# Kernel optimization log

Hardware: AMD Instinct MI355X
Metric: run time of the kernel (lower is better)

## Reference

```python
import jax, jax.numpy as jnp
import numpy as np

B, S, E, H = 4, 2048, 1024, 16
D = E // H  # head dim


def setup_inputs() -> dict:
    key = jax.random.key(0)
    ks = jax.random.split(key, 6)
    sc = 1.0 / np.sqrt(E)
    return {
        "x":  jax.random.normal(ks[0], (B, S, E), dtype=jnp.float32),
        "Wk": jax.random.normal(ks[1], (E, E), dtype=jnp.float32) * sc,
        "Wq": jax.random.normal(ks[2], (E, E), dtype=jnp.float32) * sc,
        "Wv": jax.random.normal(ks[3], (E, E), dtype=jnp.float32) * sc,
        "Wo": jax.random.normal(ks[4], (E, E), dtype=jnp.float32) * sc,
        "bo": jax.random.normal(ks[5], (E,), dtype=jnp.float32) * sc,
    }


def reference(x, Wk, Wq, Wv, Wo, bo):
    b, s, e = x.shape
    # torch Linear: y = x @ W.T (weights are [out, in])
    K = x @ Wk.T
    Q = x @ Wq.T
    _V_unused = x @ Wv.T  # computed in source but discarded (V = Q.view bug)
    # split heads: [b, s, H, D] -> [b, H, s, D]
    Kh = K.reshape(b, s, H, D).transpose(0, 2, 1, 3)
    Qh = Q.reshape(b, s, H, D).transpose(0, 2, 1, 3)
    Vh = Qh  # faithful to source: V = Q.view(...)
    # scaled dot product, scaled by sqrt(embedding_size) as in source
    scores = jnp.einsum('bhqd,bhkd->bhqk', Qh, Kh) / jnp.sqrt(jnp.float32(e))
    causal = jnp.tril(jnp.ones((s, s), dtype=bool))
    scores = jnp.where(causal, scores, -jnp.inf)
    probs = jax.nn.softmax(scores, axis=-1)
    attn = jnp.einsum('bhqk,bhkd->bhqd', probs, Vh)
    attn = attn.transpose(0, 2, 1, 3).reshape(b, s, e)
    return attn @ Wo.T + bo
```

## Files before the change

### kernel.cpp

```cpp
#include <hip/hip_runtime.h>
#include <hip/hip_bf16.h>

#define PB 4
#define PS 2048
#define PE 1024
#define PH 16
#define PD 64

typedef __attribute__((ext_vector_type(8))) short bf16x8;
typedef __attribute__((ext_vector_type(4))) float f32x4;
typedef const __attribute__((address_space(1))) unsigned int* gas_t;
typedef __attribute__((address_space(3))) unsigned int* las_t;

__device__ __forceinline__ unsigned short f2bf(float f) {
  union { float f; unsigned int u; } v;
  v.f = f;
  unsigned int u = v.u;
  u += 0x7fffu + ((u >> 16) & 1u);
  return (unsigned short)(u >> 16);
}

__device__ __forceinline__ f32x4 mfma16(bf16x8 a, bf16x8 b, f32x4 c) {
  return __builtin_amdgcn_mfma_f32_16x16x32_bf16(a, b, c, 0, 0, 0);
}

#define CVT_GROUPS ((PB * PS * PE + 3 * PE * PE) / 4)
#define CVT_BLOCKS (CVT_GROUPS / 256)
__global__ __launch_bounds__(256) void cvt_kernel(
    const float* __restrict__ x, const float* __restrict__ wk,
    const float* __restrict__ wq, const float* __restrict__ wo,
    unsigned short* __restrict__ xb, unsigned short* __restrict__ wkb,
    unsigned short* __restrict__ wqb, unsigned short* __restrict__ wob) {
  const long long NX = (long long)PB * PS * PE;
  const long long NW = (long long)PE * PE;
  long long i = ((long long)blockIdx.x * 256 + threadIdx.x) * 4;
  const float* src;
  unsigned short* dst;
  long long off;
  if (i < NX)               { src = x;  dst = xb;  off = i; }
  else if (i < NX + NW)     { src = wk; dst = wkb; off = i - NX; }
  else if (i < NX + 2 * NW) { src = wq; dst = wqb; off = i - NX - NW; }
  else                      { src = wo; dst = wob; off = i - NX - 2 * NW; }
  float4 v = *(const float4*)(src + off);
  ushort4 o;
  o.x = f2bf(v.x); o.y = f2bf(v.y); o.z = f2bf(v.z); o.w = f2bf(v.w);
  *(ushort4*)(dst + off) = o;
}

__global__ __launch_bounds__(256) void gemm_qknt(
    const unsigned short* __restrict__ A, const unsigned short* __restrict__ Bq,
    const unsigned short* __restrict__ Bk,
    unsigned short* __restrict__ QT, unsigned short* __restrict__ Kb) {
  const int K = PE, N = PE;
  __shared__ __attribute__((aligned(16))) unsigned short As[128 * 64];
  __shared__ __attribute__((aligned(16))) unsigned short Bs[128 * 64];
  const int tid = threadIdx.x;
  const int wave = tid >> 6, lane = tid & 63;
  const int quad = lane >> 4, ln = lane & 15;
  const int m0 = blockIdx.y * 128, n0 = blockIdx.x * 128;
  const int wm = (wave >> 1) * 64, wn = (wave & 1) * 64;
  const int isK = blockIdx.z;
  const unsigned short* __restrict__ Bsrc = isK ? Bk : Bq;

  f32x4 acc[4][4];
#pragma unroll
  for (int i = 0; i < 4; ++i)
#pragma unroll
    for (int j = 0; j < 4; ++j)
#pragma unroll
      for (int r = 0; r < 4; ++r) acc[i][j][r] = 0.f;

  for (int k0 = 0; k0 < K; k0 += 64) {
#pragma unroll
    for (int it = 0; it < 4; ++it) {
      const int idx = it * 256 + tid;
      const int row = idx >> 3, ch = idx & 7;
      const int gch = ch ^ (row & 7);
      __builtin_amdgcn_global_load_lds(
          (gas_t)(const void*)(A + (size_t)(m0 + row) * K + k0 + gch * 8),
          (las_t)(void*)((char*)As + idx * 16), 16, 0, 0);
      __builtin_amdgcn_global_load_lds(
          (gas_t)(const void*)(Bsrc + (size_t)(n0 + row) * K + k0 + gch * 8),
          (las_t)(void*)((char*)Bs + idx * 16), 16, 0, 0);
    }
    __syncthreads();
#pragma unroll
    for (int kc = 0; kc < 2; ++kc) {
      bf16x8 af[4], bfr[4];
#pragma unroll
      for (int t = 0; t < 4; ++t) {
        const int ra = wm + t * 16 + ln;
        const int rb = wn + t * 16 + ln;
        af[t]  = *(const bf16x8*)(As + ra * 64 + ((kc * 4 + quad) ^ (ra & 7)) * 8);
        bfr[t] = *(const bf16x8*)(Bs + rb * 64 + ((kc * 4 + quad) ^ (rb & 7)) * 8);
      }
      if (!isK) {
#pragma unroll
        for (int mt = 0; mt < 4; ++mt)
#pragma unroll
          for (int nt = 0; nt < 4; ++nt)
            acc[mt][nt] = mfma16(af[mt], bfr[nt], acc[mt][nt]);
      } else {
#pragma unroll
        for (int mt = 0; mt < 4; ++mt)
#pragma unroll
          for (int nt = 0; nt < 4; ++nt)
            acc[mt][nt] = mfma16(bfr[nt], af[mt], acc[mt][nt]);
      }
    }
    __syncthreads();
  }

  const float CEXP = 0.045084220f;
  if (!isK) {
#pragma unroll
    for (int mt = 0; mt < 4; ++mt)
#pragma unroll
      for (int nt = 0; nt < 4; ++nt) {
        const int row = m0 + wm + mt * 16 + quad * 4;
        const int col = n0 + wn + nt * 16 + ln;
        const int b = row >> 11, s = row & 2047;
        const int h = col >> 6, d = col & 63;
        ushort4 ov;
        ov.x = f2bf(acc[mt][nt][0]); ov.y = f2bf(acc[mt][nt][1]);
        ov.z = f2bf(acc[mt][nt][2]); ov.w = f2bf(acc[mt][nt][3]);
        *(ushort4*)(QT + (((size_t)(b * PH + h) * PD + d) * PS + s)) = ov;
      }
  } else {
#pragma unroll
    for (int mt = 0; mt < 4; ++mt)
#pragma unroll
      for (int nt = 0; nt < 4; ++nt) {
        const int krow = m0 + wm + mt * 16 + ln;
        const int kcol = n0 + wn + nt * 16 + quad * 4;
        ushort4 kv;
        kv.x = f2bf(acc[mt][nt][0] * CEXP); kv.y = f2bf(acc[mt][nt][1] * CEXP);
        kv.z = f2bf(acc[mt][nt][2] * CEXP); kv.w = f2bf(acc[mt][nt][3] * CEXP);
        *(ushort4*)(Kb + (size_t)krow * N + kcol) = kv;
      }
  }
}

__global__ __launch_bounds__(256) void gemm_out(
    const unsigned short* __restrict__ A, const unsigned short* __restrict__ Bm,
    const float* __restrict__ bias, float* __restrict__ Cf) {
  const int K = PE, N = PE;
  __shared__ __attribute__((aligned(16))) unsigned short As[64 * 64];
  __shared__ __attribute__((aligned(16))) unsigned short Bs[128 * 64];
  const int tid = threadIdx.x;
  const int wave = tid >> 6, lane = tid & 63;
  const int quad = lane >> 4, ln = lane & 15;
  const int m0 = blockIdx.y * 64, n0 = blockIdx.x * 128;
  const int wm = (wave >> 1) * 32, wn = (wave & 1) * 64;

  f32x4 acc[2][4];
#pragma unroll
  for (int i = 0; i < 2; ++i)
#pragma unroll
    for (int j = 0; j < 4; ++j)
#pragma unroll
      for (int r = 0; r < 4; ++r) acc[i][j][r] = 0.f;

  for (int k0 = 0; k0 < K; k0 += 64) {
#pragma unroll
    for (int it = 0; it < 2; ++it) {
      const int idx = it * 256 + tid;
      const int row = idx >> 3, ch = idx & 7;
      const int gch = ch ^ (row & 7);
      __builtin_amdgcn_global_load_lds(
          (gas_t)(const void*)(A + (size_t)(m0 + row) * K + k0 + gch * 8),
          (las_t)(void*)((char*)As + idx * 16), 16, 0, 0);
    }
#pragma unroll
    for (int it = 0; it < 4; ++it) {
      const int idx = it * 256 + tid;
      const int row = idx >> 3, ch = idx & 7;
      const int gch = ch ^ (row & 7);
      __builtin_amdgcn_global_load_lds(
          (gas_t)(const void*)(Bm + (size_t)(n0 + row) * K + k0 + gch * 8),
          (las_t)(void*)((char*)Bs + idx * 16), 16, 0, 0);
    }
    __syncthreads();
#pragma unroll
    for (int kc = 0; kc < 2; ++kc) {
      bf16x8 af[2], bfr[4];
#pragma unroll
      for (int t = 0; t < 2; ++t) {
        const int ra = wm + t * 16 + ln;
        af[t] = *(const bf16x8*)(As + ra * 64 + ((kc * 4 + quad) ^ (ra & 7)) * 8);
      }
#pragma unroll
      for (int t = 0; t < 4; ++t) {
        const int rb = wn + t * 16 + ln;
        bfr[t] = *(const bf16x8*)(Bs + rb * 64 + ((kc * 4 + quad) ^ (rb & 7)) * 8);
      }
#pragma unroll
      for (int mt = 0; mt < 2; ++mt)
#pragma unroll
        for (int nt = 0; nt < 4; ++nt)
          acc[mt][nt] = mfma16(bfr[nt], af[mt], acc[mt][nt]);
    }
    __syncthreads();
  }

#pragma unroll
  for (int mt = 0; mt < 2; ++mt) {
#pragma unroll
    for (int nt = 0; nt < 4; ++nt) {
      const int row  = m0 + wm + mt * 16 + ln;
      const int colb = n0 + wn + nt * 16 + quad * 4;
      const float4 bv = *(const float4*)(bias + colb);
      float4 ov;
      ov.x = acc[mt][nt][0] + bv.x; ov.y = acc[mt][nt][1] + bv.y;
      ov.z = acc[mt][nt][2] + bv.z; ov.w = acc[mt][nt][3] + bv.w;
      *(float4*)(Cf + (size_t)row * N + colb) = ov;
    }
  }
}

__global__ __launch_bounds__(256) void attn_kernel(
    const unsigned short* __restrict__ QT,
    const unsigned short* __restrict__ Kb,
    unsigned short* __restrict__ Ab) {
  __shared__ __attribute__((aligned(16))) unsigned short Ks[64 * 64];
  __shared__ __attribute__((aligned(16))) unsigned short Vs[64 * 64];
  __shared__ __attribute__((aligned(16))) unsigned short Ps[4][16 * 72];

  const int tid = threadIdx.x;
  const int wave = tid >> 6, lane = tid & 63;
  const int quad = lane >> 4, ln = lane & 15;
  const int h = blockIdx.y, b = blockIdx.z;
  const size_t hoff  = ((size_t)b * PS) * PE + (size_t)h * PD;
  const size_t hofft = ((size_t)(b * PH + h) * PD) * PS;
  const int srow = tid >> 3, sch = tid & 7;

  for (int pass = 0; pass < 2; ++pass) {
    const int qc = pass ? (int)blockIdx.x : 31 - (int)blockIdx.x;
    const int qw0 = qc * 64 + wave * 16;

    bf16x8 qfr[2];
#pragma unroll
    for (int c = 0; c < 2; ++c) {
      union { unsigned short u[8]; bf16x8 v; } tmp;
#pragma unroll
      for (int j = 0; j < 8; ++j)
        tmp.u[j] = QT[hofft + (size_t)(c * 32 + quad * 8 + j) * PS + qw0 + ln];
      qfr[c] = tmp.v;
    }

    f32x4 o[4];
    float psum = 0.f;
#pragma unroll
    for (int td = 0; td < 4; ++td)
#pragma unroll
      for (int r = 0; r < 4; ++r) o[td][r] = 0.f;

    const int ktend = qc + 1;
    for (int kt = 0; kt < ktend; ++kt) {
      const int k0 = kt * 64;

#pragma unroll
      for (int r = 0; r < 2; ++r) {
        const int row = r * 32 + srow;
        const int gch = sch ^ (row & 7);
        __builtin_amdgcn_global_load_lds(
            (gas_t)(const void*)(Kb + hoff + (size_t)(k0 + row) * PE + gch * 8),
            (las_t)(void*)((char*)Ks + (r * 256 + tid) * 16), 16, 0, 0);
        __builtin_amdgcn_global_load_lds(
            (gas_t)(const void*)(QT + hofft + (size_t)row * PS + k0 + gch * 8),
            (las_t)(void*)((char*)Vs + (r * 256 + tid) * 16), 16, 0, 0);
      }
      __syncthreads();

      f32x4 sacc[4];
#pragma unroll
      for (int mk = 0; mk < 4; ++mk)
#pragma unroll
        for (int r = 0; r < 4; ++r) sacc[mk][r] = 0.f;
      __builtin_amdgcn_s_setprio(1);
#pragma unroll
      for (int c = 0; c < 2; ++c) {
        const int ch = ((c * 4 + quad) ^ (ln & 7)) * 8;
        bf16x8 kf[4];
#pragma unroll
        for (int mk = 0; mk < 4; ++mk)
          kf[mk] = *(const bf16x8*)(Ks + (mk * 16 + ln) * 64 + ch);
#pragma unroll
        for (int mk = 0; mk < 4; ++mk)
          sacc[mk] = mfma16(kf[mk], qfr[c], sacc[mk]);
      }
      __builtin_amdgcn_s_setprio(0);

      const bool edge = (k0 + 63) > qw0;
#pragma unroll
      for (int mk = 0; mk < 4; ++mk) {
        float p[4];
#pragma unroll
        for (int r = 0; r < 4; ++r)
          p[r] = __builtin_amdgcn_exp2f(sacc[mk][r]);
        if (edge) {
          const int qg = qw0 + ln;
#pragma unroll
          for (int r = 0; r < 4; ++r) {
            const int kg = k0 + mk * 16 + quad * 4 + r;
            p[r] = (kg <= qg) ? p[r] : 0.f;
          }
        }
        psum += (p[0] + p[1]) + (p[2] + p[3]);
        union { __hip_bfloat162 h2; unsigned int u; } u01, u23;
        u01.h2 = __float22bfloat162_rn(float2{p[0], p[1]});
        u23.h2 = __float22bfloat162_rn(float2{p[2], p[3]});
        *(uint2*)(&Ps[wave][ln * 72 + mk * 16 + quad * 4]) =
            uint2{u01.u, u23.u};
      }

      __builtin_amdgcn_s_setprio(1);
#pragma unroll
      for (int c = 0; c < 2; ++c) {
        const int ch = ((c * 4 + quad) ^ (ln & 7)) * 8;
        bf16x8 pf = *(const bf16x8*)(&Ps[wave][ln * 72 + c * 32 + quad * 8]);
#pragma unroll
        for (int td = 0; td < 4; ++td) {
          bf16x8 vfd = *(const bf16x8*)(Vs + (td * 16 + ln) * 64 + ch);
          o[td] = mfma16(pf, vfd, o[td]);
        }
      }
      __builtin_amdgcn_s_setprio(0);
      __syncthreads();
    }

    psum += __shfl_xor(psum, 16, 64);
    psum += __shfl_xor(psum, 32, 64);
    float invq[4];
#pragma unroll
    for (int r = 0; r < 4; ++r)
      invq[r] = 1.f / __shfl(psum, quad * 4 + r, 64);

#pragma unroll
    for (int r = 0; r < 4; ++r) {
      const int qg = qw0 + quad * 4 + r;
#pragma unroll
      for (int td = 0; td < 4; ++td)
        Ab[hoff + (size_t)qg * PE + td * 16 + ln] =
            f2bf(o[td][r] * invq[r]);
    }
  }
}

extern "C" void kernel_launch(void* const* d_in, const int* in_sizes, int n_in,
                              void* d_out, int out_size, void* d_ws, size_t ws_size,
                              hipStream_t stream) {
  (void)in_sizes; (void)n_in; (void)out_size; (void)ws_size;
  const float* x  = (const float*)d_in[0];
  const float* Wk = (const float*)d_in[1];
  const float* Wq = (const float*)d_in[2];
  const float* Wo = (const float*)d_in[4];
  const float* bo = (const float*)d_in[5];
  float* out = (float*)d_out;

  char* ws = (char*)d_ws;
  unsigned short* xb  = (unsigned short*)(ws);
  unsigned short* wkb = (unsigned short*)(ws + (16u << 20));
  unsigned short* wqb = (unsigned short*)(ws + (18u << 20));
  unsigned short* wob = (unsigned short*)(ws + (20u << 20));
  unsigned short* QT  = (unsigned short*)(ws + (22u << 20));
  unsigned short* Kb  = (unsigned short*)(ws + (38u << 20));
  unsigned short* Ab  = xb;

  const int M = PB * PS;

  cvt_kernel<<<dim3(CVT_BLOCKS), dim3(256), 0, stream>>>(
      x, Wk, Wq, Wo, xb, wkb, wqb, wob);

  gemm_qknt<<<dim3(PE / 128, M / 128, 2), dim3(256), 0, stream>>>(
      xb, wqb, wkb, QT, Kb);

  attn_kernel<<<dim3(16, PH, PB), dim3(256), 0, stream>>>(QT, Kb, Ab);

  gemm_out<<<dim3(PE / 128, M / 64), dim3(256), 0, stream>>>(
      Ab, wob, bo, out);
}
```

Measured before the change: 246.4 us.

## Restructure attention around 32x32 MFMA with split-K waves and register P

The attention kernel moves from 16x16x32 MFMA tiles to 32x32x16 tiles. The four waves are arranged as 2 query groups by 2 key halves, and the two key-half partial outputs and row sums are reduced through LDS at the end. The P matrix is handed to the PV MFMA through register lane shuffles instead of a per-wave LDS round trip, and waves whose key half is fully masked skip their work. It also remaps block indices to group heads for L2 locality and sets launch bounds to 4 blocks per CU, at the cost of an extra cross-wave reduction and synchronisation per pass.

```diff
diff --git a/kernel.cpp b/kernel.cpp
--- a/kernel.cpp
+++ b/kernel.cpp
@@ -9,6 +9,7 @@
 
 typedef __attribute__((ext_vector_type(8))) short bf16x8;
 typedef __attribute__((ext_vector_type(4))) float f32x4;
+typedef __attribute__((ext_vector_type(16))) float f32x16;
 typedef const __attribute__((address_space(1))) unsigned int* gas_t;
 typedef __attribute__((address_space(3))) unsigned int* las_t;
 
@@ -22,6 +23,10 @@
 
 __device__ __forceinline__ f32x4 mfma16(bf16x8 a, bf16x8 b, f32x4 c) {
   return __builtin_amdgcn_mfma_f32_16x16x32_bf16(a, b, c, 0, 0, 0);
+}
+
+__device__ __forceinline__ f32x16 mfma32(bf16x8 a, bf16x8 b, f32x16 c) {
+  return __builtin_amdgcn_mfma_f32_32x32x16_bf16(a, b, c, 0, 0, 0);
 }
 
 #define CVT_GROUPS ((PB * PS * PE + 3 * PE * PE) / 4)
@@ -218,132 +223,163 @@
   }
 }
 
-__global__ __launch_bounds__(256) void attn_kernel(
+__global__ __launch_bounds__(256, 4) void attn_kernel(
     const unsigned short* __restrict__ QT,
     const unsigned short* __restrict__ Kb,
     unsigned short* __restrict__ Ab) {
-  __shared__ __attribute__((aligned(16))) unsigned short Ks[64 * 64];
-  __shared__ __attribute__((aligned(16))) unsigned short Vs[64 * 64];
-  __shared__ __attribute__((aligned(16))) unsigned short Ps[4][16 * 72];
+  __shared__ __attribute__((aligned(16))) char smem[16384 + 512];
+  unsigned short* Ks = (unsigned short*)smem;
+  unsigned short* Vs = (unsigned short*)(smem + 8192);
+  float* om    = (float*)smem;
+  float* psLds = (float*)(smem + 16384);
 
   const int tid = threadIdx.x;
   const int wave = tid >> 6, lane = tid & 63;
-  const int quad = lane >> 4, ln = lane & 15;
-  const int h = blockIdx.y, b = blockIdx.z;
+  const int wq = wave >> 1, wk = wave & 1;
+  const int lq = lane & 31, hi = lane >> 5;
+
+  const int fp = (int)blockIdx.x + ((int)blockIdx.y << 4) + ((int)blockIdx.z << 8);
+  const int xr = fp & 7, sl = fp >> 3;
+  const int bx = sl & 15;
+  const int g  = ((sl >> 4) << 3) + xr;
+  const int h = g & 15, b = g >> 4;
+
   const size_t hoff  = ((size_t)b * PS) * PE + (size_t)h * PD;
   const size_t hofft = ((size_t)(b * PH + h) * PD) * PS;
-  const int srow = tid >> 3, sch = tid & 7;
 
   for (int pass = 0; pass < 2; ++pass) {
-    const int qc = pass ? (int)blockIdx.x : 31 - (int)blockIdx.x;
-    const int qw0 = qc * 64 + wave * 16;
-
-    bf16x8 qfr[2];
-#pragma unroll
-    for (int c = 0; c < 2; ++c) {
-      union { unsigned short u[8]; bf16x8 v; } tmp;
+    const int qc = pass ? bx : 31 - bx;
+    const int qw0 = qc * 64 + wq * 32;
+    const int qg = qw0 + lq;
+
+    bf16x8 qfr[4];
+#pragma unroll
+    for (int s4 = 0; s4 < 4; ++s4) {
+      union { unsigned short u[8]; bf16x8 v; } t;
 #pragma unroll
       for (int j = 0; j < 8; ++j)
-        tmp.u[j] = QT[hofft + (size_t)(c * 32 + quad * 8 + j) * PS + qw0 + ln];
-      qfr[c] = tmp.v;
-    }
-
-    f32x4 o[4];
+        t.u[j] = QT[hofft + (size_t)(16 * s4 + 8 * hi + j) * PS + qg];
+      qfr[s4] = t.v;
+    }
+
+    f32x16 o0, o1;
+#pragma unroll
+    for (int i = 0; i < 16; ++i) { o0[i] = 0.f; o1[i] = 0.f; }
     float psum = 0.f;
-#pragma unroll
-    for (int td = 0; td < 4; ++td)
-#pragma unroll
-      for (int r = 0; r < 4; ++r) o[td][r] = 0.f;
 
     const int ktend = qc + 1;
     for (int kt = 0; kt < ktend; ++kt) {
       const int k0 = kt * 64;
 
 #pragma unroll
-      for (int r = 0; r < 2; ++r) {
-        const int row = r * 32 + srow;
-        const int gch = sch ^ (row & 7);
+      for (int it = 0; it < 2; ++it) {
+        const int idx = it * 256 + tid;
+        const int row = idx >> 3, ch = idx & 7;
+        const int gch = ch ^ (row & 7);
         __builtin_amdgcn_global_load_lds(
             (gas_t)(const void*)(Kb + hoff + (size_t)(k0 + row) * PE + gch * 8),
-            (las_t)(void*)((char*)Ks + (r * 256 + tid) * 16), 16, 0, 0);
+            (las_t)(void*)((char*)Ks + idx * 16), 16, 0, 0);
         __builtin_amdgcn_global_load_lds(
             (gas_t)(const void*)(QT + hofft + (size_t)row * PS + k0 + gch * 8),
-            (las_t)(void*)((char*)Vs + (r * 256 + tid) * 16), 16, 0, 0);
+            (las_t)(void*)((char*)Vs + idx * 16), 16, 0, 0);
       }
       __syncthreads();
 
-      f32x4 sacc[4];
-#pragma unroll
-      for (int mk = 0; mk < 4; ++mk)
-#pragma unroll
-        for (int r = 0; r < 4; ++r) sacc[mk][r] = 0.f;
-      __builtin_amdgcn_s_setprio(1);
-#pragma unroll
-      for (int c = 0; c < 2; ++c) {
-        const int ch = ((c * 4 + quad) ^ (ln & 7)) * 8;
-        bf16x8 kf[4];
-#pragma unroll
-        for (int mk = 0; mk < 4; ++mk)
-          kf[mk] = *(const bf16x8*)(Ks + (mk * 16 + ln) * 64 + ch);
-#pragma unroll
-        for (int mk = 0; mk < 4; ++mk)
-          sacc[mk] = mfma16(kf[mk], qfr[c], sacc[mk]);
-      }
-      __builtin_amdgcn_s_setprio(0);
-
-      const bool edge = (k0 + 63) > qw0;
-#pragma unroll
-      for (int mk = 0; mk < 4; ++mk) {
-        float p[4];
-#pragma unroll
-        for (int r = 0; r < 4; ++r)
-          p[r] = __builtin_amdgcn_exp2f(sacc[mk][r]);
-        if (edge) {
-          const int qg = qw0 + ln;
-#pragma unroll
-          for (int r = 0; r < 4; ++r) {
-            const int kg = k0 + mk * 16 + quad * 4 + r;
-            p[r] = (kg <= qg) ? p[r] : 0.f;
+      const int kbw = k0 + wk * 32;
+      if (kbw <= qw0 + 31) {
+        f32x16 sacc;
+#pragma unroll
+        for (int i = 0; i < 16; ++i) sacc[i] = 0.f;
+        const int krow = wk * 32 + lq;
+        __builtin_amdgcn_s_setprio(1);
+#pragma unroll
+        for (int s4 = 0; s4 < 4; ++s4) {
+          const int ch = ((2 * s4 + hi) ^ (krow & 7)) * 8;
+          bf16x8 kf = *(const bf16x8*)(Ks + krow * 64 + ch);
+          sacc = mfma32(kf, qfr[s4], sacc);
+        }
+        __builtin_amdgcn_s_setprio(0);
+
+        const bool edge = (kbw + 31) > qw0;
+        const int kb4 = kbw + 4 * hi;
+#pragma unroll
+        for (int sb = 0; sb < 2; ++sb) {
+          float pv[8];
+#pragma unroll
+          for (int i = 0; i < 8; ++i) {
+            float e = __builtin_amdgcn_exp2f(sacc[8 * sb + i]);
+            if (edge) {
+              const int kg = kb4 + (i & 3) + 8 * (2 * sb + (i >> 2));
+              e = (kg <= qg) ? e : 0.f;
+            }
+            pv[i] = e;
           }
+          psum += ((pv[0] + pv[1]) + (pv[2] + pv[3])) +
+                  ((pv[4] + pv[5]) + (pv[6] + pv[7]));
+          union { __hip_bfloat162 h2; unsigned int u; } c0, c1, c2, c3;
+          c0.h2 = __float22bfloat162_rn(float2{pv[0], pv[1]});
+          c1.h2 = __float22bfloat162_rn(float2{pv[2], pv[3]});
+          c2.h2 = __float22bfloat162_rn(float2{pv[4], pv[5]});
+          c3.h2 = __float22bfloat162_rn(float2{pv[6], pv[7]});
+          const unsigned int e0 = (unsigned int)__shfl_xor((int)c0.u, 32, 64);
+          const unsigned int e1 = (unsigned int)__shfl_xor((int)c1.u, 32, 64);
+          const unsigned int e2 = (unsigned int)__shfl_xor((int)c2.u, 32, 64);
+          const unsigned int e3 = (unsigned int)__shfl_xor((int)c3.u, 32, 64);
+          union { unsigned int u[4]; bf16x8 v; } pf;
+          pf.u[0] = hi ? e2 : c0.u;
+          pf.u[1] = hi ? e3 : c1.u;
+          pf.u[2] = hi ? c2.u : e0;
+          pf.u[3] = hi ? c3.u : e1;
+
+          const int chv = wk * 4 + 2 * sb + hi;
+          __builtin_amdgcn_s_setprio(1);
+          {
+            const int r0 = lq;
+            bf16x8 vf0 = *(const bf16x8*)(Vs + r0 * 64 + ((chv ^ (r0 & 7)) * 8));
+            o0 = mfma32(pf.v, vf0, o0);
+            const int r1 = 32 + lq;
+            bf16x8 vf1 = *(const bf16x8*)(Vs + r1 * 64 + ((chv ^ (r1 & 7)) * 8));
+            o1 = mfma32(pf.v, vf1, o1);
+          }
+          __builtin_amdgcn_s_setprio(0);
         }
-        psum += (p[0] + p[1]) + (p[2] + p[3]);
-        union { __hip_bfloat162 h2; unsigned int u; } u01, u23;
-        u01.h2 = __float22bfloat162_rn(float2{p[0], p[1]});
-        u23.h2 = __float22bfloat162_rn(float2{p[2], p[3]});
-        *(uint2*)(&Ps[wave][ln * 72 + mk * 16 + quad * 4]) =
-            uint2{u01.u, u23.u};
-      }
-
-      __builtin_amdgcn_s_setprio(1);
-#pragma unroll
-      for (int c = 0; c < 2; ++c) {
-        const int ch = ((c * 4 + quad) ^ (ln & 7)) * 8;
-        bf16x8 pf = *(const bf16x8*)(&Ps[wave][ln * 72 + c * 32 + quad * 8]);
-#pragma unroll
-        for (int td = 0; td < 4; ++td) {
-          bf16x8 vfd = *(const bf16x8*)(Vs + (td * 16 + ln) * 64 + ch);
-          o[td] = mfma16(pf, vfd, o[td]);
-        }
-      }
-      __builtin_amdgcn_s_setprio(0);
+      }
       __syncthreads();
     }
 
-    psum += __shfl_xor(psum, 16, 64);
     psum += __shfl_xor(psum, 32, 64);
-    float invq[4];
-#pragma unroll
-    for (int r = 0; r < 4; ++r)
-      invq[r] = 1.f / __shfl(psum, quad * 4 + r, 64);
-
-#pragma unroll
-    for (int r = 0; r < 4; ++r) {
-      const int qg = qw0 + quad * 4 + r;
-#pragma unroll
-      for (int td = 0; td < 4; ++td)
-        Ab[hoff + (size_t)qg * PE + td * 16 + ln] =
-            f2bf(o[td][r] * invq[r]);
-    }
+    if (lane < 32) psLds[(wq * 2 + wk) * 32 + lane] = psum;
+    if (wk == 1) {
+#pragma unroll
+      for (int c = 0; c < 8; ++c) {
+        const int base = (c & 3) * 4;
+        float4 v;
+        if (c < 4) v = float4{o0[base], o0[base + 1], o0[base + 2], o0[base + 3]};
+        else       v = float4{o1[base], o1[base + 1], o1[base + 2], o1[base + 3]};
+        *(float4*)(om + ((wq * 8 + c) * 64 + lane) * 4) = v;
+      }
+    }
+    __syncthreads();
+    if (wk == 0) {
+#pragma unroll
+      for (int c = 0; c < 8; ++c) {
+        const float4 v = *(const float4*)(om + ((wq * 8 + c) * 64 + lane) * 4);
+        const int base = (c & 3) * 4;
+        if (c < 4) { o0[base] += v.x; o0[base+1] += v.y; o0[base+2] += v.z; o0[base+3] += v.w; }
+        else       { o1[base] += v.x; o1[base+1] += v.y; o1[base+2] += v.z; o1[base+3] += v.w; }
+      }
+#pragma unroll
+      for (int reg = 0; reg < 16; ++reg) {
+        const int qrow = (reg & 3) + 8 * (reg >> 2) + 4 * hi;
+        const float tot = psLds[(wq * 2 + 0) * 32 + qrow] +
+                          psLds[(wq * 2 + 1) * 32 + qrow];
+        const float inv = 1.f / tot;
+        const size_t rb = hoff + (size_t)(qw0 + qrow) * PE;
+        Ab[rb + lq]      = f2bf(o0[reg] * inv);
+        Ab[rb + 32 + lq] = f2bf(o1[reg] * inv);
+      }
+    }
+    __syncthreads();
   }
 }
 
@@ -375,7 +411,7 @@
   gemm_qknt<<<dim3(PE / 128, M / 128, 2), dim3(256), 0, stream>>>(
       xb, wqb, wkb, QT, Kb);
 
-  attn_kernel<<<dim3(16, PH, PB), dim3(256), 0, stream>>>(QT, Kb, Ab);
+  attn_kernel<<<dim3(16, 16, 4), dim3(256), 0, stream>>>(QT, Kb, Ab);
 
   gemm_out<<<dim3(PE / 128, M / 64), dim3(256), 0, stream>>>(
       Ab, wob, bo, out);
```

Result: no change. 250.3 us (+1.6%).
